# Kernel optimization log

Hardware: AMD Instinct MI355X
Metric: run time of the kernel (lower is better)

## Reference

```python
import jax, jax.numpy as jnp
import numpy as np

V_TH = 1.0       # IFNode default threshold
SG_ALPHA = 4.0   # spikingjelly Sigmoid surrogate default alpha


def _spike(v):
    # Heaviside forward, sigmoid surrogate gradient (straight-through)
    sur = jax.nn.sigmoid(SG_ALPHA * (v - V_TH))
    hard = (v >= V_TH).astype(v.dtype)
    return sur + jax.lax.stop_gradient(hard - sur)


def setup_inputs() -> dict:
    key = jax.random.key(0)
    k1, k2, k3 = jax.random.split(key, 3)
    T, B, IN, H, OUT = 32, 1024, 784, 4096, 10
    x_seq = jax.random.uniform(k1, (T, B, IN), dtype=jnp.float32)
    W1 = jax.random.normal(k2, (H, IN), dtype=jnp.float32) * 0.05
    W2 = jax.random.normal(k3, (OUT, H), dtype=jnp.float32) * 0.05
    return {"x_seq": x_seq, "W1": W1, "W2": W2}


def reference(x_seq, W1, W2):
    T, B = x_seq.shape[0], x_seq.shape[1]
    x = x_seq.reshape(T, B, -1)  # [T, B, in_dim]
    H, OUT = W1.shape[0], W2.shape[0]

    def step(carry, xt):
        v1, v2, rec = carry
        v1 = v1 + xt @ W1.T          # integrate layer 1
        s1 = _spike(v1)
        v1 = v1 * (1.0 - s1)         # hard reset to v_reset=0
        v2 = v2 + s1 @ W2.T          # integrate layer 2
        s2 = _spike(v2)
        v2 = v2 * (1.0 - s2)
        return (v1, v2, rec + s2), None

    init = (jnp.zeros((B, H), x_seq.dtype),
            jnp.zeros((B, OUT), x_seq.dtype),
            jnp.zeros((B, OUT), x_seq.dtype))
    (v1, v2, spike_record), _ = jax.lax.scan(step, init, x)
    return spike_record  # [B, OUTPUT_NEURONS]
```

## Files before the change

### kernel.cpp

```cpp
#include <hip/hip_runtime.h>
#include <stdint.h>

typedef __attribute__((ext_vector_type(8))) short bf16x8;
typedef __attribute__((ext_vector_type(4))) float f32x4;

#define T_TOTAL 32
#define BATCH   1024
#define INDIM   784
#define HDIM    4096
#define OUTDIM  10
#define BH      (BATCH * HDIM)
#define WORDS_PER_T (BH / 64)
#define TC      8
#define MC      (TC * BATCH)
#define KP      2368
#define DELTA   2e-3f
#define FIXLIST 3072

__device__ __forceinline__ void split2(float a, ushort& h, ushort& m) {
    unsigned ua = __float_as_uint(a);
    h = (ushort)(ua >> 16);
    float r = a - __uint_as_float(ua & 0xFFFF0000u);
    m = (ushort)(__float_as_uint(r) >> 16);
}

__global__ __launch_bounds__(256) void k_split3(const float* __restrict__ src,
                                                ushort* __restrict__ dst,
                                                int R, int isA) {
    int idx = blockIdx.x * 256 + threadIdx.x;
    int main_n = R * 392;
    if (idx < main_n) {
        int row = idx / 392, kk = (idx % 392) * 2;
        float a0 = src[(size_t)row * INDIM + kk];
        float a1 = src[(size_t)row * INDIM + kk + 1];
        ushort h0, m0, h1, m1;
        split2(a0, h0, m0);
        split2(a1, h1, m1);
        ushort2 H; H.x = h0; H.y = h1;
        ushort2 M; M.x = m0; M.y = m1;
        ushort2 s1 = isA ? H : M;
        ushort2 s2 = isA ? M : H;
        ushort* d = dst + (size_t)row * KP;
        *(ushort2*)(d + kk)        = s1;
        *(ushort2*)(d + 784 + kk)  = s2;
        *(ushort2*)(d + 1568 + kk) = H;
    } else if (idx < main_n + R * 8) {
        int j = idx - main_n;
        int row = j / 8, q = j % 8;
        ushort2 z; z.x = 0; z.y = 0;
        *(ushort2*)(dst + (size_t)row * KP + 2352 + q * 2) = z;
    }
}

__global__ void k_transpose_w2(const float* __restrict__ W2, float* __restrict__ W2T) {
    int i = blockIdx.x * 256 + threadIdx.x;
    if (i < HDIM * OUTDIM) {
        int h = i / OUTDIM, o = i % OUTDIM;
        W2T[i] = W2[o * HDIM + h];
    }
}

__global__ __launch_bounds__(256) void k_gemm_bf16(const ushort* __restrict__ Ap,
                                                   const ushort* __restrict__ Bp,
                                                   float* __restrict__ Z) {
    __shared__ ushort Asm[128 * 64];
    __shared__ ushort Bsm[128 * 64];

    const int nwg = gridDim.x;
    const int cpx = nwg >> 3;
    const int bid = blockIdx.x;
    const int swz = (bid & 7) * cpx + (bid >> 3);
    const int bm = swz >> 5;
    const int bn = swz & 31;

    const int tid  = threadIdx.x;
    const int w    = tid >> 6, lane = tid & 63;
    const int wr   = w >> 1,   wc   = w & 1;
    const int fr   = lane & 15, fq  = lane >> 4;

    const ushort* agbase = Ap + ((size_t)(bm * 128 + w * 32 + (lane >> 3))) * KP + (lane & 7) * 8;
    const ushort* bgbase = Bp + ((size_t)(bn * 128 + w * 32 + (lane >> 3))) * KP + (lane & 7) * 8;
    ushort* alds = &Asm[(w * 32) * 64];
    ushort* blds = &Bsm[(w * 32) * 64];

    f32x4 acc[4][4];
#pragma unroll
    for (int i = 0; i < 4; ++i)
#pragma unroll
        for (int j = 0; j < 4; ++j) acc[i][j] = (f32x4){0.f, 0.f, 0.f, 0.f};

    const bf16x8* As8 = (const bf16x8*)Asm;
    const bf16x8* Bs8 = (const bf16x8*)Bsm;
    const int aoff = (wr * 64 + fr) * 8 + fq;
    const int boff = (wc * 64 + fr) * 8 + fq;

    for (int k0 = 0; k0 < KP; k0 += 64) {
#pragma unroll
        for (int i = 0; i < 4; ++i) {
            __builtin_amdgcn_global_load_lds(
                (const __attribute__((address_space(1))) void*)(agbase + (size_t)i * 8 * KP + k0),
                (__attribute__((address_space(3))) void*)(alds + i * 8 * 64), 16, 0, 0);
            __builtin_amdgcn_global_load_lds(
                (const __attribute__((address_space(1))) void*)(bgbase + (size_t)i * 8 * KP + k0),
                (__attribute__((address_space(3))) void*)(blds + i * 8 * 64), 16, 0, 0);
        }
        __syncthreads();
#pragma unroll
        for (int kk = 0; kk < 2; ++kk) {
            bf16x8 a0 = As8[aoff + kk * 4 + 0 * 128];
            bf16x8 a1 = As8[aoff + kk * 4 + 1 * 128];
            bf16x8 a2 = As8[aoff + kk * 4 + 2 * 128];
            bf16x8 a3 = As8[aoff + kk * 4 + 3 * 128];
            bf16x8 b0 = Bs8[boff + kk * 4 + 0 * 128];
            bf16x8 b1 = Bs8[boff + kk * 4 + 1 * 128];
            bf16x8 b2 = Bs8[boff + kk * 4 + 2 * 128];
            bf16x8 b3 = Bs8[boff + kk * 4 + 3 * 128];
            acc[0][0] = __builtin_amdgcn_mfma_f32_16x16x32_bf16(a0, b0, acc[0][0], 0, 0, 0);
            acc[0][1] = __builtin_amdgcn_mfma_f32_16x16x32_bf16(a0, b1, acc[0][1], 0, 0, 0);
            acc[0][2] = __builtin_amdgcn_mfma_f32_16x16x32_bf16(a0, b2, acc[0][2], 0, 0, 0);
            acc[0][3] = __builtin_amdgcn_mfma_f32_16x16x32_bf16(a0, b3, acc[0][3], 0, 0, 0);
            acc[1][0] = __builtin_amdgcn_mfma_f32_16x16x32_bf16(a1, b0, acc[1][0], 0, 0, 0);
            acc[1][1] = __builtin_amdgcn_mfma_f32_16x16x32_bf16(a1, b1, acc[1][1], 0, 0, 0);
            acc[1][2] = __builtin_amdgcn_mfma_f32_16x16x32_bf16(a1, b2, acc[1][2], 0, 0, 0);
            acc[1][3] = __builtin_amdgcn_mfma_f32_16x16x32_bf16(a1, b3, acc[1][3], 0, 0, 0);
            acc[2][0] = __builtin_amdgcn_mfma_f32_16x16x32_bf16(a2, b0, acc[2][0], 0, 0, 0);
            acc[2][1] = __builtin_amdgcn_mfma_f32_16x16x32_bf16(a2, b1, acc[2][1], 0, 0, 0);
            acc[2][2] = __builtin_amdgcn_mfma_f32_16x16x32_bf16(a2, b2, acc[2][2], 0, 0, 0);
            acc[2][3] = __builtin_amdgcn_mfma_f32_16x16x32_bf16(a2, b3, acc[2][3], 0, 0, 0);
            acc[3][0] = __builtin_amdgcn_mfma_f32_16x16x32_bf16(a3, b0, acc[3][0], 0, 0, 0);
            acc[3][1] = __builtin_amdgcn_mfma_f32_16x16x32_bf16(a3, b1, acc[3][1], 0, 0, 0);
            acc[3][2] = __builtin_amdgcn_mfma_f32_16x16x32_bf16(a3, b2, acc[3][2], 0, 0, 0);
            acc[3][3] = __builtin_amdgcn_mfma_f32_16x16x32_bf16(a3, b3, acc[3][3], 0, 0, 0);
        }
        __syncthreads();
    }

    const int mbase = bm * 128 + wr * 64 + fq * 4;
    const int nbase = bn * 128 + wc * 64 + fr;
#pragma unroll
    for (int i = 0; i < 4; ++i)
#pragma unroll
        for (int j = 0; j < 4; ++j)
#pragma unroll
            for (int r = 0; r < 4; ++r)
                Z[(size_t)(mbase + i * 16 + r) * HDIM + nbase + j * 16] = acc[i][j][r];
}

__global__ __launch_bounds__(256) void k_layer1_flag(const float* __restrict__ Z,
                                                     float* __restrict__ v1s,
                                                     uint64_t* __restrict__ S1,
                                                     uint64_t* __restrict__ flags,
                                                     int tbase, int first) {
    const size_t i = (size_t)blockIdx.x * 256 + threadIdx.x;
    float v = first ? 0.0f : v1s[i];
    const int lane = threadIdx.x & 63;
    const size_t word = i >> 6;
    uint64_t nearAcc = 0;
    for (int t = 0; t < TC; ++t) {
        v += Z[(size_t)t * BH + i];
        bool s    = (v >= 1.0f);
        bool near = (fabsf(v - 1.0f) < DELTA);
        unsigned long long sm = __ballot(s);
        nearAcc |= (uint64_t)__ballot(near);
        if (lane == 0) S1[(size_t)(tbase + t) * WORDS_PER_T + word] = sm;
        if (s) v = 0.0f;
    }
    if (lane == 0) flags[word] = first ? nearAcc : (flags[word] | nearAcc);
    v1s[i] = v;
}

__global__ __launch_bounds__(256) void k_fixup(const float* __restrict__ x,
                                               const float* __restrict__ W1,
                                               const uint64_t* __restrict__ flags,
                                               uint64_t* __restrict__ S1) {
    __shared__ float xs[16][788];
    __shared__ int   list[FIXLIST];
    __shared__ int   cnt;
    const int b   = blockIdx.x;
    const int tid = threadIdx.x;
    if (tid == 0) cnt = 0;
    __syncthreads();
    if (tid < 64) {
        uint64_t w = flags[b * 64 + tid];
        while (w) {
            int bit = __builtin_ctzll(w);
            w &= w - 1;
            int p = atomicAdd(&cnt, 1);
            if (p < FIXLIST) list[p] = tid * 64 + bit;
        }
    }
    __syncthreads();
    const int n = min(cnt, FIXLIST);
    if (n == 0) return;

    for (int j0 = 0; j0 < n; j0 += 256) {
        const int j = j0 + tid;
        const int h = (j < n) ? list[j] : -1;
        const float* wrow = W1 + (size_t)(h >= 0 ? h : 0) * INDIM;
        float v = 0.0f;
        for (int half = 0; half < 2; ++half) {
            __syncthreads();
            for (int idx = tid; idx < 16 * 196; idx += 256) {
                int t  = idx / 196;
                int kq = (idx % 196) * 4;
                float4 vx = *(const float4*)(x + ((size_t)(half * 16 + t) * BATCH + b) * INDIM + kq);
                *(float4*)&xs[t][kq] = vx;
            }
            __syncthreads();
            if (h >= 0) {
                float z[16];
#pragma unroll
                for (int t = 0; t < 16; ++t) z[t] = 0.0f;
                for (int kq = 0; kq < INDIM; kq += 4) {
                    float4 w4 = *(const float4*)(wrow + kq);
#pragma unroll
                    for (int t = 0; t < 16; ++t) {
                        float4 xv = *(const float4*)&xs[t][kq];
                        z[t] = fmaf(xv.x, w4.x, z[t]);
                        z[t] = fmaf(xv.y, w4.y, z[t]);
                        z[t] = fmaf(xv.z, w4.z, z[t]);
                        z[t] = fmaf(xv.w, w4.w, z[t]);
                    }
                }
#pragma unroll
                for (int t = 0; t < 16; ++t) {
                    v += z[t];
                    bool s = (v >= 1.0f);
                    unsigned long long* wp = (unsigned long long*)
                        &S1[(size_t)(half * 16 + t) * WORDS_PER_T + (size_t)b * 64 + (h >> 6)];
                    unsigned long long m = 1ull << (h & 63);
                    if (s) { atomicOr(wp, m); v = 0.0f; }
                    else   { atomicAnd(wp, ~m); }
                }
            }
        }
    }
}

__global__ __launch_bounds__(256) void k_layer2_partial(const uint64_t* __restrict__ S1,
                                                        const float* __restrict__ W2T,
                                                        float* __restrict__ part,
                                                        int rowsTotal) {
    __shared__ float w[1024][10];
    const int hs = blockIdx.y;
    for (int i = threadIdx.x; i < 1024 * 10; i += 256)
        w[i / 10][i % 10] = W2T[hs * 1024 * 10 + i];
    __syncthreads();

    const int row = blockIdx.x * 256 + threadIdx.x;
    const uint64_t* wp = S1 + (size_t)row * 64 + hs * 16;
    float acc[10] = {};
    for (int wi = 0; wi < 16; ++wi) {
        uint64_t m = wp[wi];
        while (m) {
            int bit = __builtin_ctzll(m);
            m &= m - 1;
            int hl = wi * 64 + bit;
#pragma unroll
            for (int o = 0; o < 10; ++o) acc[o] += w[hl][o];
        }
    }
    float* p = part + ((size_t)hs * rowsTotal + row) * 10;
#pragma unroll
    for (int o = 0; o < 10; ++o) p[o] = acc[o];
}

__global__ __launch_bounds__(256) void k_layer2_rec(const float* __restrict__ part,
                                                    float* __restrict__ out) {
    const int i = blockIdx.x * 256 + threadIdx.x;
    if (i >= BATCH * OUTDIM) return;
    float v = 0.0f, rec = 0.0f;
    const int rowsTotal = T_TOTAL * BATCH;
    const int b = i / OUTDIM, o = i % OUTDIM;
    for (int t = 0; t < T_TOTAL; ++t) {
        const int r = t * BATCH + b;
        float sig = 0.0f;
#pragma unroll
        for (int hs = 0; hs < 4; ++hs)
            sig += part[((size_t)hs * rowsTotal + r) * 10 + o];
        v += sig;
        bool s = (v >= 1.0f);
        rec += s ? 1.0f : 0.0f;
        if (s) v = 0.0f;
    }
    out[i] = rec;
}

extern "C" void kernel_launch(void* const* d_in, const int* in_sizes, int n_in,
                              void* d_out, int out_size, void* d_ws, size_t ws_size,
                              hipStream_t stream) {
    (void)in_sizes; (void)n_in; (void)out_size; (void)ws_size;
    const float* x  = (const float*)d_in[0];
    const float* W1 = (const float*)d_in[1];
    const float* W2 = (const float*)d_in[2];
    float* out = (float*)d_out;

    char* p = (char*)d_ws;
    float*    W2T   = (float*)p;    p += (size_t)HDIM * OUTDIM * 4;
    float*    v1s   = (float*)p;    p += (size_t)BH * 4;
    ushort*   Bp    = (ushort*)p;   p += (size_t)HDIM * KP * 2;
    ushort*   Ap    = (ushort*)p;   p += (size_t)MC * KP * 2;
    float*    Z     = (float*)p;    p += (size_t)TC * BH * 4;
    uint64_t* S1    = (uint64_t*)p; p += (size_t)T_TOTAL * WORDS_PER_T * 8;
    uint64_t* flags = (uint64_t*)p; p += (size_t)WORDS_PER_T * 8;
    float*    part  = (float*)p;

    k_transpose_w2<<<(HDIM * OUTDIM + 255) / 256, 256, 0, stream>>>(W2, W2T);
    k_split3<<<(HDIM * 400 + 255) / 256, 256, 0, stream>>>(W1, Bp, HDIM, 0);

    const int nch = T_TOTAL / TC;
    for (int c = 0; c < nch; ++c) {
        const float* xc = x + (size_t)c * MC * INDIM;
        k_split3<<<(MC * 400 + 255) / 256, 256, 0, stream>>>(xc, Ap, MC, 1);
        k_gemm_bf16<<<(MC / 128) * 32, 256, 0, stream>>>(Ap, Bp, Z);
        k_layer1_flag<<<BH / 256, 256, 0, stream>>>(Z, v1s, S1, flags, c * TC, c == 0);
    }
    k_fixup<<<BATCH, 256, 0, stream>>>(x, W1, flags, S1);
    k_layer2_partial<<<dim3(T_TOTAL * BATCH / 256, 4), 256, 0, stream>>>(
        S1, W2T, part, T_TOTAL * BATCH);
    k_layer2_rec<<<(BATCH * OUTDIM + 255) / 256, 256, 0, stream>>>(part, out);
}
```

Before: 1.508 ms.

## Rewrite bf16 GEMM with 256x256 tiles, 512 threads and double-buffered LDS

The layer-1 GEMM moves from a 128x128 tile with 256 threads and a single LDS buffer to a 256x256 tile with 8 waves, K-step 32 and two LDS buffers. Global-to-LDS loads for the next K slice are issued while MFMAs run, split into two halves with barriers between them, and s_setprio raises wave priority around the MFMA blocks. The aim is to hide memory latency and raise the amount of compute done per byte loaded. The cost is more accumulator registers per thread, which may lower occupancy, and hand-tuned vmcnt waits that must match the order in which loads are issued.

```diff
diff --git a/kernel.cpp b/kernel.cpp
--- a/kernel.cpp
+++ b/kernel.cpp
@@ -14,6 +14,7 @@
 #define TC      8
 #define MC      (TC * BATCH)
 #define KP      2368
+#define NT      74
 #define DELTA   2e-3f
 #define FIXLIST 3072
 
@@ -60,90 +61,105 @@
     }
 }
 
-__global__ __launch_bounds__(256) void k_gemm_bf16(const ushort* __restrict__ Ap,
+__global__ __launch_bounds__(512) void k_gemm_bf16(const ushort* __restrict__ Ap,
                                                    const ushort* __restrict__ Bp,
                                                    float* __restrict__ Z) {
-    __shared__ ushort Asm[128 * 64];
-    __shared__ ushort Bsm[128 * 64];
-
-    const int nwg = gridDim.x;
-    const int cpx = nwg >> 3;
-    const int bid = blockIdx.x;
-    const int swz = (bid & 7) * cpx + (bid >> 3);
-    const int bm = swz >> 5;
-    const int bn = swz & 31;
+    __shared__ ushort Asm[2][256 * 32];
+    __shared__ ushort Bsm[2][256 * 32];
+
+    const int cpx = gridDim.x >> 3;
+    const int swz = (blockIdx.x & 7) * cpx + (blockIdx.x >> 3);
+    const int bm  = swz >> 4;
+    const int bn  = swz & 15;
 
     const int tid  = threadIdx.x;
-    const int w    = tid >> 6, lane = tid & 63;
-    const int wr   = w >> 1,   wc   = w & 1;
-    const int fr   = lane & 15, fq  = lane >> 4;
-
-    const ushort* agbase = Ap + ((size_t)(bm * 128 + w * 32 + (lane >> 3))) * KP + (lane & 7) * 8;
-    const ushort* bgbase = Bp + ((size_t)(bn * 128 + w * 32 + (lane >> 3))) * KP + (lane & 7) * 8;
-    ushort* alds = &Asm[(w * 32) * 64];
-    ushort* blds = &Bsm[(w * 32) * 64];
-
-    f32x4 acc[4][4];
-#pragma unroll
-    for (int i = 0; i < 4; ++i)
+    const int wid  = tid >> 6, lane = tid & 63;
+    const int wm   = wid >> 2, wn = wid & 3;
+    const int fr   = lane & 15, fq = lane >> 4;
+
+    const int srow  = tid >> 2;
+    const int skcol = (tid & 3) << 3;
+    const ushort* agb = Ap + (size_t)(bm * 256 + srow) * KP + skcol;
+    const ushort* bgb = Bp + (size_t)(bn * 256 + srow) * KP + skcol;
+    const int sbase = wid * 16 * 32;
+
+#define STAGE_A(t, s) do {                                                            \
+    __builtin_amdgcn_global_load_lds(                                                 \
+        (const __attribute__((address_space(1))) void*)(agb + (size_t)(t) * 32),      \
+        (__attribute__((address_space(3))) void*)(&Asm[s][sbase]), 16, 0, 0);         \
+    __builtin_amdgcn_global_load_lds(                                                 \
+        (const __attribute__((address_space(1))) void*)(agb + (size_t)(t) * 32 + (size_t)128 * KP), \
+        (__attribute__((address_space(3))) void*)(&Asm[s][4096 + sbase]), 16, 0, 0);  \
+} while (0)
+#define STAGE_B(t, s) do {                                                            \
+    __builtin_amdgcn_global_load_lds(                                                 \
+        (const __attribute__((address_space(1))) void*)(bgb + (size_t)(t) * 32),      \
+        (__attribute__((address_space(3))) void*)(&Bsm[s][sbase]), 16, 0, 0);         \
+    __builtin_amdgcn_global_load_lds(                                                 \
+        (const __attribute__((address_space(1))) void*)(bgb + (size_t)(t) * 32 + (size_t)128 * KP), \
+        (__attribute__((address_space(3))) void*)(&Bsm[s][4096 + sbase]), 16, 0, 0);  \
+} while (0)
+
+    f32x4 acc[8][4];
+#pragma unroll
+    for (int i = 0; i < 8; ++i)
 #pragma unroll
         for (int j = 0; j < 4; ++j) acc[i][j] = (f32x4){0.f, 0.f, 0.f, 0.f};
 
-    const bf16x8* As8 = (const bf16x8*)Asm;
-    const bf16x8* Bs8 = (const bf16x8*)Bsm;
-    const int aoff = (wr * 64 + fr) * 8 + fq;
-    const int boff = (wc * 64 + fr) * 8 + fq;
-
-    for (int k0 = 0; k0 < KP; k0 += 64) {
-#pragma unroll
-        for (int i = 0; i < 4; ++i) {
-            __builtin_amdgcn_global_load_lds(
-                (const __attribute__((address_space(1))) void*)(agbase + (size_t)i * 8 * KP + k0),
-                (__attribute__((address_space(3))) void*)(alds + i * 8 * 64), 16, 0, 0);
-            __builtin_amdgcn_global_load_lds(
-                (const __attribute__((address_space(1))) void*)(bgbase + (size_t)i * 8 * KP + k0),
-                (__attribute__((address_space(3))) void*)(blds + i * 8 * 64), 16, 0, 0);
-        }
-        __syncthreads();
-#pragma unroll
-        for (int kk = 0; kk < 2; ++kk) {
-            bf16x8 a0 = As8[aoff + kk * 4 + 0 * 128];
-            bf16x8 a1 = As8[aoff + kk * 4 + 1 * 128];
-            bf16x8 a2 = As8[aoff + kk * 4 + 2 * 128];
-            bf16x8 a3 = As8[aoff + kk * 4 + 3 * 128];
-            bf16x8 b0 = Bs8[boff + kk * 4 + 0 * 128];
-            bf16x8 b1 = Bs8[boff + kk * 4 + 1 * 128];
-            bf16x8 b2 = Bs8[boff + kk * 4 + 2 * 128];
-            bf16x8 b3 = Bs8[boff + kk * 4 + 3 * 128];
-            acc[0][0] = __builtin_amdgcn_mfma_f32_16x16x32_bf16(a0, b0, acc[0][0], 0, 0, 0);
-            acc[0][1] = __builtin_amdgcn_mfma_f32_16x16x32_bf16(a0, b1, acc[0][1], 0, 0, 0);
-            acc[0][2] = __builtin_amdgcn_mfma_f32_16x16x32_bf16(a0, b2, acc[0][2], 0, 0, 0);
-            acc[0][3] = __builtin_amdgcn_mfma_f32_16x16x32_bf16(a0, b3, acc[0][3], 0, 0, 0);
-            acc[1][0] = __builtin_amdgcn_mfma_f32_16x16x32_bf16(a1, b0, acc[1][0], 0, 0, 0);
-            acc[1][1] = __builtin_amdgcn_mfma_f32_16x16x32_bf16(a1, b1, acc[1][1], 0, 0, 0);
-            acc[1][2] = __builtin_amdgcn_mfma_f32_16x16x32_bf16(a1, b2, acc[1][2], 0, 0, 0);
-            acc[1][3] = __builtin_amdgcn_mfma_f32_16x16x32_bf16(a1, b3, acc[1][3], 0, 0, 0);
-            acc[2][0] = __builtin_amdgcn_mfma_f32_16x16x32_bf16(a2, b0, acc[2][0], 0, 0, 0);
-            acc[2][1] = __builtin_amdgcn_mfma_f32_16x16x32_bf16(a2, b1, acc[2][1], 0, 0, 0);
-            acc[2][2] = __builtin_amdgcn_mfma_f32_16x16x32_bf16(a2, b2, acc[2][2], 0, 0, 0);
-            acc[2][3] = __builtin_amdgcn_mfma_f32_16x16x32_bf16(a2, b3, acc[2][3], 0, 0, 0);
-            acc[3][0] = __builtin_amdgcn_mfma_f32_16x16x32_bf16(a3, b0, acc[3][0], 0, 0, 0);
-            acc[3][1] = __builtin_amdgcn_mfma_f32_16x16x32_bf16(a3, b1, acc[3][1], 0, 0, 0);
-            acc[3][2] = __builtin_amdgcn_mfma_f32_16x16x32_bf16(a3, b2, acc[3][2], 0, 0, 0);
-            acc[3][3] = __builtin_amdgcn_mfma_f32_16x16x32_bf16(a3, b3, acc[3][3], 0, 0, 0);
-        }
-        __syncthreads();
-    }
-
-    const int mbase = bm * 128 + wr * 64 + fq * 4;
-    const int nbase = bn * 128 + wc * 64 + fr;
-#pragma unroll
-    for (int i = 0; i < 4; ++i)
+    const int aidx = (wm * 128 + fr) * 4 + fq;
+    const int bidx = (wn * 64 + fr) * 4 + fq;
+
+    STAGE_A(0, 0);
+    STAGE_B(0, 0);
+    STAGE_A(1, 1);
+
+    for (int t = 0; t < NT; ++t) {
+        const int s = t & 1;
+        if (t == NT - 1) asm volatile("s_waitcnt vmcnt(0)" ::: "memory");
+        else             asm volatile("s_waitcnt vmcnt(2)" ::: "memory");
+        __builtin_amdgcn_s_barrier();
+
+        const bf16x8* A8 = (const bf16x8*)Asm[s];
+        const bf16x8* B8 = (const bf16x8*)Bsm[s];
+
+        bf16x8 fa[8];
+#pragma unroll
+        for (int i = 0; i < 8; ++i) fa[i] = A8[aidx + i * 64];
+        bf16x8 fb0 = B8[bidx];
+        bf16x8 fb1 = B8[bidx + 64];
+        if (t + 1 < NT) STAGE_B(t + 1, s ^ 1);
+        __builtin_amdgcn_s_setprio(1);
+#pragma unroll
+        for (int i = 0; i < 8; ++i) {
+            acc[i][0] = __builtin_amdgcn_mfma_f32_16x16x32_bf16(fa[i], fb0, acc[i][0], 0, 0, 0);
+            acc[i][1] = __builtin_amdgcn_mfma_f32_16x16x32_bf16(fa[i], fb1, acc[i][1], 0, 0, 0);
+        }
+        __builtin_amdgcn_s_setprio(0);
+
+        __builtin_amdgcn_s_barrier();
+        if (t + 2 < NT) STAGE_A(t + 2, s);
+        bf16x8 fb2 = B8[bidx + 128];
+        bf16x8 fb3 = B8[bidx + 192];
+        __builtin_amdgcn_s_setprio(1);
+#pragma unroll
+        for (int i = 0; i < 8; ++i) {
+            acc[i][2] = __builtin_amdgcn_mfma_f32_16x16x32_bf16(fa[i], fb2, acc[i][2], 0, 0, 0);
+            acc[i][3] = __builtin_amdgcn_mfma_f32_16x16x32_bf16(fa[i], fb3, acc[i][3], 0, 0, 0);
+        }
+        __builtin_amdgcn_s_setprio(0);
+    }
+
+    const int m0 = bm * 256 + wm * 128 + fq * 4;
+    const int n0 = bn * 256 + wn * 64 + fr;
+#pragma unroll
+    for (int i = 0; i < 8; ++i)
 #pragma unroll
         for (int j = 0; j < 4; ++j)
 #pragma unroll
             for (int r = 0; r < 4; ++r)
-                Z[(size_t)(mbase + i * 16 + r) * HDIM + nbase + j * 16] = acc[i][j][r];
+                Z[(size_t)(m0 + i * 16 + r) * HDIM + n0 + j * 16] = acc[i][j][r];
+#undef STAGE_A
+#undef STAGE_B
 }
 
 __global__ __launch_bounds__(256) void k_layer1_flag(const float* __restrict__ Z,
@@ -203,8 +219,8 @@
             for (int idx = tid; idx < 16 * 196; idx += 256) {
                 int t  = idx / 196;
                 int kq = (idx % 196) * 4;
-                float4 vx = *(const float4*)(x + ((size_t)(half * 16 + t) * BATCH + b) * INDIM + kq);
-                *(float4*)&xs[t][kq] = vx;
+                *(float4*)&xs[t][kq] =
+                    *(const float4*)(x + ((size_t)(half * 16 + t) * BATCH + b) * INDIM + kq);
             }
             __syncthreads();
             if (h >= 0) {
@@ -312,7 +328,7 @@
     for (int c = 0; c < nch; ++c) {
         const float* xc = x + (size_t)c * MC * INDIM;
         k_split3<<<(MC * 400 + 255) / 256, 256, 0, stream>>>(xc, Ap, MC, 1);
-        k_gemm_bf16<<<(MC / 128) * 32, 256, 0, stream>>>(Ap, Bp, Z);
+        k_gemm_bf16<<<(MC / 256) * (HDIM / 256), 512, 0, stream>>>(Ap, Bp, Z);
         k_layer1_flag<<<BH / 256, 256, 0, stream>>>(Z, v1s, S1, flags, c * TC, c == 0);
     }
     k_fixup<<<BATCH, 256, 0, stream>>>(x, W1, flags, S1);
```

Result: faster. 1.314 ms (-12.9%).
